# Kernel tuning notes

Measured on AMD Instinct MI355X. Metric: run time of the kernel, lower is better.

## Reference

```python
import jax, jax.numpy as jnp
import numpy as np

EPS = 1e-5

def _rms(t, w):
    # RMSNorm over last dim with learned scale w (broadcastable)
    return t * jax.lax.rsqrt(jnp.mean(t * t, axis=-1, keepdims=True) + EPS) * w

def setup_inputs() -> dict:
    key = jax.random.key(0)
    ks = jax.random.split(key, 8)
    B, S, D, H, HD, M = 2, 2048, 1024, 16, 64, 2
    E = H * HD
    sc = 0.02
    x = jax.random.normal(ks[0], (B, S, D), jnp.float32)
    attn_mask = jnp.zeros((S, S), jnp.float32)  # additive mask
    mod_ids = jax.random.randint(ks[1], (B, S), 0, M)
    Wq = jax.random.normal(ks[2], (M, D, E), jnp.float32) * sc
    Wk = jax.random.normal(ks[3], (M, D, E), jnp.float32) * sc
    Wv = jax.random.normal(ks[4], (M, D, E), jnp.float32) * sc
    Wo = jax.random.normal(ks[5], (M, E, D), jnp.float32) * sc
    qn_w = jnp.ones((M, HD), jnp.float32)
    kn_w = jnp.ones((M, HD), jnp.float32)
    attn_norm_w = jnp.ones((M, D), jnp.float32)
    return {"x": x, "attn_mask": attn_mask, "mod_ids": mod_ids,
            "Wq": Wq, "Wk": Wk, "Wv": Wv, "Wo": Wo,
            "qn_w": qn_w, "kn_w": kn_w, "attn_norm_w": attn_norm_w}

def reference(x, attn_mask, mod_ids, Wq, Wk, Wv, Wo, qn_w, kn_w, attn_norm_w):
    B, S, D = x.shape
    M = Wq.shape[0]
    HD = qn_w.shape[-1]
    E = Wq.shape[-1]
    H = E // HD
    msk = jax.nn.one_hot(mod_ids, M, dtype=x.dtype)  # [B,S,M] one-hot routing

    # modality-expert QKV projections: [M,B,S,E]
    q_m = jnp.einsum('bsd,mde->mbse', x, Wq).reshape(M, B, S, H, HD)
    k_m = jnp.einsum('bsd,mde->mbse', x, Wk).reshape(M, B, S, H, HD)
    v_m = jnp.einsum('bsd,mde->mbse', x, Wv)
    # per-modality, per-head QK RMSNorm
    q_m = _rms(q_m, qn_w[:, None, None, None, :]).reshape(M, B, S, E)
    k_m = _rms(k_m, kn_w[:, None, None, None, :]).reshape(M, B, S, E)

    # merge modalities (scatter by routing mask)
    q = jnp.einsum('bsm,mbse->bse', msk, q_m).reshape(B, S, H, HD)
    k = jnp.einsum('bsm,mbse->bse', msk, k_m).reshape(B, S, H, HD)
    v = jnp.einsum('bsm,mbse->bse', msk, v_m).reshape(B, S, H, HD)

    # standard multi-head attention
    scores = jnp.einsum('bqhd,bkhd->bhqk', q, k) / jnp.sqrt(jnp.asarray(HD, x.dtype))
    scores = scores + attn_mask  # additive mask broadcast over [B,H]
    attn = jax.nn.softmax(scores, axis=-1)
    ctx = jnp.einsum('bhqk,bkhd->bqhd', attn, v).reshape(B, S, E)
    attn_weights = attn.mean(axis=1)  # [B,S,S], averaged over heads

    # modality-expert output projection + RMSNorm, scatter-merge back
    o_m = jnp.einsum('bse,med->mbsd', ctx, Wo)
    o_m = _rms(o_m, attn_norm_w[:, None, None, :])
    out = jnp.einsum('bsm,mbsd->bsd', msk, o_m)
    return out, attn_weights
```

## Files before the change

kernel.cpp:

```cpp
#include <hip/hip_runtime.h>
#include <cstdint>

#define Bc  2
#define Sc  2048
#define Dc  1024
#define Ec  1024
#define Hc  16
#define HDc 64
#define TTc (Bc*Sc)
#define TILE_R 128
#define NTILES 36
#define EPSc 1e-5f
#define LOG2E 1.44269504f
#define C2    (0.125f*LOG2E)

typedef unsigned short u16;
using bf8   = __attribute__((ext_vector_type(8))) short;
using f32x4 = __attribute__((ext_vector_type(4))) float;
#define MFMA(a,b,c) __builtin_amdgcn_mfma_f32_16x16x32_bf16(a,b,c,0,0,0)

static __device__ __forceinline__ u16 f2b(float f){
    return (u16)((__float_as_uint(f) + 0x8000u) >> 16);
}
static __device__ __forceinline__ float b2f(u16 s){
    return __uint_as_float(((unsigned)s) << 16);
}
static __device__ __forceinline__ float ex2(float x){
    return __builtin_amdgcn_exp2f(x);
}
static __device__ __forceinline__ unsigned cvtpk(float a, float b){
    unsigned r;
    asm("v_cvt_pk_bf16_f32 %0, %1, %2" : "=v"(r) : "v"(a), "v"(b));
    return r;
}
union bfpack { unsigned u[4]; bf8 v; };
static __device__ __forceinline__ u16* swz(u16* base, int row, int col8){
    return base + row*64 + ((col8 ^ (row & 7)) << 3);
}
static __device__ __forceinline__ const u16* swzc(const u16* base, int row, int col8){
    return base + row*64 + ((col8 ^ (row & 7)) << 3);
}
typedef const __attribute__((address_space(1))) void* gp1;
typedef __attribute__((address_space(3))) void* lp3;
static __device__ __forceinline__ void gl16(const void* g, void* l){
    __builtin_amdgcn_global_load_lds((gp1)g, (lp3)l, 16, 0, 0);
}

__global__ void k_perm(const int* __restrict__ mod, int* __restrict__ perm,
                       int* __restrict__ tmeta, u16* __restrict__ zbuf)
{
    __shared__ int cnt[4], segstart[4];
    int t = threadIdx.x;
    for (int i = t; i < 2048; i += 256) zbuf[i] = 0;
    if (t < 4) cnt[t] = 0;
    __syncthreads();
    for (int i = t; i < TTc; i += 256){
        int b = i >> 11; int m = mod[i];
        atomicAdd(&cnt[b*2+m], 1);
    }
    __syncthreads();
    if (t == 0){
        int off = 0;
        for (int i = 0; i < 4; i++){
            segstart[i] = off;
            int pad = ((cnt[i] + TILE_R - 1)/TILE_R)*TILE_R;
            for (int tt = off/TILE_R; tt < (off+pad)/TILE_R; tt++) tmeta[tt] = i;
            off += pad;
        }
        for (int tt = off/TILE_R; tt < NTILES; tt++) tmeta[tt] = -1;
    }
    __syncthreads();
    if (t < 4) cnt[t] = 0;
    for (int i = t; i < NTILES*TILE_R; i += 256) perm[i] = -1;
    __syncthreads();
    for (int i = t; i < TTc; i += 256){
        int b = i >> 11, s = i & 2047; int m = mod[i];
        int r = atomicAdd(&cnt[b*2+m], 1);
        perm[segstart[b*2+m] + r] = s;
    }
}

__global__ __launch_bounds__(256) void k_f2b(const float* __restrict__ src,
                                             u16* __restrict__ dst, int n)
{
    int i = (blockIdx.x*256 + threadIdx.x)*4;
    if (i >= n) return;
    float4 v = *(const float4*)&src[i];
    ushort4 o;
    o.x = f2b(v.x); o.y = f2b(v.y); o.z = f2b(v.z); o.w = f2b(v.w);
    *(ushort4*)&dst[i] = o;
}

__global__ __launch_bounds__(256) void k_f2bs(const float* __restrict__ src,
                                              u16* __restrict__ dst, int n, float sc)
{
    int i = (blockIdx.x*256 + threadIdx.x)*4;
    if (i >= n) return;
    float4 v = *(const float4*)&src[i];
    ushort4 o;
    o.x = f2b(v.x*sc); o.y = f2b(v.y*sc); o.z = f2b(v.z*sc); o.w = f2b(v.w*sc);
    *(ushort4*)&dst[i] = o;
}

__global__ __launch_bounds__(256) void k_tcvt(
    const float* __restrict__ s0, const float* __restrict__ s1,
    const float* __restrict__ s2, const float* __restrict__ s3,
    u16* __restrict__ d0, u16* __restrict__ d1,
    u16* __restrict__ d2, u16* __restrict__ d3)
{
    int wsel = blockIdx.z >> 1, m = blockIdx.z & 1;
    const float* src = (wsel==0?s0:wsel==1?s1:wsel==2?s2:s3) + (size_t)m*1048576;
    u16*       dst = (wsel==0?d0:wsel==1?d1:wsel==2?d2:d3) + (size_t)m*1048576;
    __shared__ float sh[32][33];
    int t = threadIdx.x;
    int i0 = blockIdx.x*32, j0 = blockIdx.y*32;
    {
        int i = t >> 3, j4 = (t & 7)*4;
        *(float4*)&sh[i][j4] = *(const float4*)&src[(size_t)(i0+i)*1024 + j0 + j4];
    }
    __syncthreads();
    {
        int j = t >> 3, i4 = (t & 7)*4;
        ushort4 o;
        o.x = f2b(sh[i4+0][j]); o.y = f2b(sh[i4+1][j]);
        o.z = f2b(sh[i4+2][j]); o.w = f2b(sh[i4+3][j]);
        *(ushort4*)&dst[(size_t)(j0+j)*1024 + i0 + i4] = o;
    }
}

__global__ __launch_bounds__(256) void k_qkv(
    const u16* __restrict__ xb, const u16* __restrict__ wqT,
    const u16* __restrict__ wkT, const u16* __restrict__ wvT,
    const int* __restrict__ perm, const int* __restrict__ tmeta,
    const float* __restrict__ qnw, const float* __restrict__ knw,
    const u16* __restrict__ zbuf,
    u16* __restrict__ qb, u16* __restrict__ kb, u16* __restrict__ vb)
{
    int meta = tmeta[blockIdx.y];
    if (meta < 0) return;
    int b = meta >> 1, m = meta & 1;
    const u16* W = (blockIdx.z==0 ? wqT : (blockIdx.z==1 ? wkT : wvT)) + (size_t)m*Ec*Dc;
    u16* outp    = (blockIdx.z==0 ? qb  : (blockIdx.z==1 ? kb  : vb));
    int c0 = blockIdx.x*128;
    int t = threadIdx.x, lane = t & 63, wv_ = t >> 6;
    int quad = lane >> 4, lc = lane & 15;

    __shared__ u16 at[128*64];
    __shared__ u16 bt[128*64];
    __shared__ int sperm[128];
    if (t < 128) sperm[t] = perm[blockIdx.y*128 + t];
    f32x4 acc[2][8];
    #pragma unroll
    for (int i=0;i<2;i++)
        #pragma unroll
        for (int j=0;j<8;j++) acc[i][j] = (f32x4){0.f,0.f,0.f,0.f};
    __syncthreads();

    int colsw = ((lane & 7) ^ (lane >> 3)) << 3;
    const u16* ab[4]; const u16* bb[4];
    #pragma unroll
    for (int i = 0; i < 4; i++){
        int row = wv_*32 + i*8 + (lane >> 3);
        int s_ = sperm[row];
        ab[i] = (s_ >= 0) ? (xb + ((size_t)(b*Sc + s_))*Dc + colsw) : zbuf;
        bb[i] = W + (size_t)(c0 + row)*Dc + colsw;
    }

    for (int d0 = 0; d0 < Dc; d0 += 64){
        #pragma unroll
        for (int i = 0; i < 4; i++){
            gl16(ab[i] + d0, &at[(wv_*4 + i)*512]);
            gl16(bb[i] + d0, &bt[(wv_*4 + i)*512]);
        }
        __syncthreads();
        #pragma unroll
        for (int ks = 0; ks < 2; ks++){
            bf8 a0 = *(const bf8*)swzc(at, wv_*32 + lc,      ks*4 + quad);
            bf8 a1 = *(const bf8*)swzc(at, wv_*32 + 16 + lc, ks*4 + quad);
            #pragma unroll
            for (int nb = 0; nb < 8; nb++){
                bf8 bb2 = *(const bf8*)swzc(bt, nb*16 + lc, ks*4 + quad);
                acc[0][nb] = MFMA(a0, bb2, acc[0][nb]);
                acc[1][nb] = MFMA(a1, bb2, acc[1][nb]);
            }
        }
        __syncthreads();
    }

    if (blockIdx.z < 2){
        const float* nw = (blockIdx.z==0 ? qnw : knw) + m*HDc;
        float cs = (blockIdx.z==0) ? C2 : 1.f;
        float w0 = nw[lc]*cs, w1 = nw[16+lc]*cs, w2 = nw[32+lc]*cs, w3 = nw[48+lc]*cs;
        #pragma unroll
        for (int mb = 0; mb < 2; mb++){
            #pragma unroll
            for (int r = 0; r < 4; r++){
                #pragma unroll
                for (int g = 0; g < 2; g++){
                    float ss = 0.f;
                    #pragma unroll
                    for (int j = 0; j < 4; j++){
                        float v2 = acc[mb][g*4+j][r];
                        ss += v2*v2;
                    }
                    ss += __shfl_xor(ss, 1, 64);
                    ss += __shfl_xor(ss, 2, 64);
                    ss += __shfl_xor(ss, 4, 64);
                    ss += __shfl_xor(ss, 8, 64);
                    float rs = rsqrtf(ss*(1.f/64.f) + EPSc);
                    acc[mb][g*4+0][r] *= rs*w0;
                    acc[mb][g*4+1][r] *= rs*w1;
                    acc[mb][g*4+2][r] *= rs*w2;
                    acc[mb][g*4+3][r] *= rs*w3;
                }
            }
        }
    }

    int h0 = c0 >> 6;
    #pragma unroll
    for (int mb = 0; mb < 2; mb++){
        #pragma unroll
        for (int r = 0; r < 4; r++){
            int row = wv_*32 + mb*16 + quad*4 + r;
            int s_ = sperm[row];
            if (s_ < 0) continue;
            #pragma unroll
            for (int nb = 0; nb < 8; nb++){
                int col = nb*16 + lc;
                int h = h0 + (col >> 6), hd = col & 63;
                outp[(((size_t)(b*Hc + h))*Sc + s_)*HDc + hd] = f2b(acc[mb][nb][r]);
            }
        }
    }
}

__global__ __launch_bounds__(256) void k_vt(const u16* __restrict__ vb,
                                            u16* __restrict__ vtb)
{
    __shared__ u16 sh[64][72];
    int t = threadIdx.x;
    int s0 = blockIdx.x*64, bh = blockIdx.y;
    {
        int rr = t >> 2, cc = (t & 3)*16;
        const u16* src = vb + ((size_t)bh*Sc + s0 + rr)*HDc + cc;
        *(uint4*)&sh[rr][cc]   = *(const uint4*)(src);
        *(uint4*)&sh[rr][cc+8] = *(const uint4*)(src+8);
    }
    __syncthreads();
    {
        int hd = t >> 2, sc = (t & 3)*16;
        u16 tmp[16];
        #pragma unroll
        for (int j = 0; j < 16; j++) tmp[j] = sh[sc+j][hd];
        u16* dst = vtb + ((size_t)bh*HDc + hd)*Sc + s0 + sc;
        *(uint4*)(dst)   = *(const uint4*)&tmp[0];
        *(uint4*)(dst+8) = *(const uint4*)&tmp[8];
    }
}

__global__ __launch_bounds__(256) void k_flash(
    const u16* __restrict__ qb, const u16* __restrict__ kb,
    const u16* __restrict__ vtb, const u16* __restrict__ maskb,
    float* __restrict__ pm, float* __restrict__ pl,
    u16* __restrict__ c0, u16* __restrict__ c1)
{
    int qs0 = blockIdx.x*64, h = blockIdx.y;
    int b = blockIdx.z >> 1, half = blockIdx.z & 1;
    u16* ctxh = half ? c1 : c0;
    int t = threadIdx.x, lane = t & 63, wv_ = t >> 6;
    int quad = lane >> 4, lc = lane & 15;
    __shared__ u16 kt[64*64];
    __shared__ u16 vt[64*64];
    const u16* qp  = qb  + ((size_t)(b*Hc+h))*Sc*HDc;
    const u16* kp  = kb  + ((size_t)(b*Hc+h))*Sc*HDc;
    const u16* vtp = vtb + ((size_t)(b*Hc+h))*HDc*Sc;
    const u16* mq  = maskb + (size_t)(qs0 + wv_*16 + lc)*Sc;
    bf8 aq[2];
    #pragma unroll
    for (int ks = 0; ks < 2; ks++)
        aq[ks] = *(const bf8*)(qp + (size_t)(qs0 + wv_*16 + lc)*HDc + ks*32 + quad*8);
    float rm = -1.0e30f, rl = 0.f;
    f32x4 oacc[4];
    #pragma unroll
    for (int j=0;j<4;j++) oacc[j] = (f32x4){0.f,0.f,0.f,0.f};

    int rr = t >> 2, c8 = (t & 3)*2;
    int pr = (rr & 0x23) | ((rr & 0x04) << 2) | ((rr & 0x18) >> 1);
    int kc0 = half*1024;
    for (int kc = kc0; kc < kc0 + 1024; kc += 64){
        ushort4 mv[2][2];
        #pragma unroll
        for (int a1 = 0; a1 < 2; a1++)
            #pragma unroll
            for (int b1 = 0; b1 < 2; b1++)
                mv[a1][b1] = *(const ushort4*)(mq + kc + a1*32 + quad*8 + b1*4);
        __syncthreads();
        {
            const u16* s1 = kp + (size_t)(kc+rr)*HDc + c8*8;
            *(uint4*)swz(kt, pr, c8)   = *(const uint4*)(s1);
            *(uint4*)swz(kt, pr, c8+1) = *(const uint4*)(s1+8);
            const u16* s2 = vtp + (size_t)rr*Sc + kc + c8*8;
            *(uint4*)swz(vt, rr, c8)   = *(const uint4*)(s2);
            *(uint4*)swz(vt, rr, c8+1) = *(const uint4*)(s2+8);
        }
        __syncthreads();
        f32x4 acc[4];
        #pragma unroll
        for (int j=0;j<4;j++) acc[j] = (f32x4){0.f,0.f,0.f,0.f};
        #pragma unroll
        for (int ks = 0; ks < 2; ks++){
            #pragma unroll
            for (int nb = 0; nb < 4; nb++){
                bf8 ak = *(const bf8*)swzc(kt, nb*16 + lc, ks*4 + quad);
                acc[nb] = MFMA(ak, aq[ks], acc[nb]);
            }
        }
        float svv[4][4];
        float mxl = -3.0e38f;
        #pragma unroll
        for (int a1 = 0; a1 < 2; a1++){
            #pragma unroll
            for (int b1 = 0; b1 < 2; b1++){
                int nb = 2*a1 + b1;
                #pragma unroll
                for (int r = 0; r < 4; r++){
                    u16 mraw = (r==0?mv[a1][b1].x:r==1?mv[a1][b1].y:
                                r==2?mv[a1][b1].z:mv[a1][b1].w);
                    float s2v = acc[nb][r] + b2f(mraw);
                    svv[nb][r] = s2v;
                    mxl = fmaxf(mxl, s2v);
                }
            }
        }
        if (__any(mxl > rm + 8.f)){
            float mx = fmaxf(mxl, __shfl_xor(mxl, 16, 64));
            mx = fmaxf(mx, __shfl_xor(mx, 32, 64));
            float nm = fmaxf(rm, mx);
            float fac = ex2(rm - nm);
            rm = nm;
            rl *= fac;
            float f0 = __shfl(fac, quad*4+0, 64);
            float f1 = __shfl(fac, quad*4+1, 64);
            float f2 = __shfl(fac, quad*4+2, 64);
            float f3 = __shfl(fac, quad*4+3, 64);
            #pragma unroll
            for (int nb = 0; nb < 4; nb++){
                oacc[nb][0] *= f0; oacc[nb][1] *= f1;
                oacc[nb][2] *= f2; oacc[nb][3] *= f3;
            }
        }
        #pragma unroll
        for (int a1 = 0; a1 < 2; a1++){
            bfpack pk;
            {
                float p0 = ex2(svv[2*a1][0] - rm);
                float p1 = ex2(svv[2*a1][1] - rm);
                float p2 = ex2(svv[2*a1][2] - rm);
                float p3 = ex2(svv[2*a1][3] - rm);
                rl += (p0 + p1) + (p2 + p3);
                pk.u[0] = cvtpk(p0, p1); pk.u[1] = cvtpk(p2, p3);
            }
            {
                float p0 = ex2(svv[2*a1+1][0] - rm);
                float p1 = ex2(svv[2*a1+1][1] - rm);
                float p2 = ex2(svv[2*a1+1][2] - rm);
                float p3 = ex2(svv[2*a1+1][3] - rm);
                rl += (p0 + p1) + (p2 + p3);
                pk.u[2] = cvtpk(p0, p1); pk.u[3] = cvtpk(p2, p3);
            }
            bf8 ap = pk.v;
            #pragma unroll
            for (int nb2 = 0; nb2 < 4; nb2++){
                bf8 bv = *(const bf8*)swzc(vt, nb2*16 + lc, a1*4 + quad);
                oacc[nb2] = MFMA(ap, bv, oacc[nb2]);
            }
        }
    }
    rl += __shfl_xor(rl, 16, 64);
    rl += __shfl_xor(rl, 32, 64);
    if (quad == 0){
        size_t srow = ((size_t)(b*Hc+h))*Sc + qs0 + wv_*16 + lc;
        pm[(size_t)half*65536 + srow] = rm;
        pl[(size_t)half*65536 + srow] = rl;
    }
    float i0 = 1.f/__shfl(rl, quad*4+0, 64);
    float i1 = 1.f/__shfl(rl, quad*4+1, 64);
    float i2 = 1.f/__shfl(rl, quad*4+2, 64);
    float i3 = 1.f/__shfl(rl, quad*4+3, 64);
    #pragma unroll
    for (int r = 0; r < 4; r++){
        float ir = (r==0?i0:r==1?i1:r==2?i2:i3);
        int tok = qs0 + wv_*16 + quad*4 + r;
        #pragma unroll
        for (int nb = 0; nb < 4; nb++){
            int hd = nb*16 + lc;
            ctxh[((size_t)(b*Sc + tok))*Ec + h*HDc + hd] = f2b(oacc[nb][r]*ir);
        }
    }
}

__global__ __launch_bounds__(256) void k_merge(
    const float* __restrict__ pm, const float* __restrict__ pl,
    float* __restrict__ lstc, float* __restrict__ w0, float* __restrict__ w1)
{
    int r = blockIdx.x*256 + threadIdx.x;
    float m0 = pm[r],        m1 = pm[65536 + r];
    float l0 = pl[r],        l1 = pl[65536 + r];
    float M  = fmaxf(m0, m1);
    float e0 = ex2(m0 - M)*l0;
    float e1 = ex2(m1 - M)*l1;
    float L  = e0 + e1;
    float iL = 1.f/L;
    lstc[r] = M + log2f(L);
    w0[r] = e0*iL;
    w1[r] = e1*iL;
}

__global__ __launch_bounds__(256) void k_addc(u16* __restrict__ c0,
                                              const u16* __restrict__ c1,
                                              const float* __restrict__ w0,
                                              const float* __restrict__ w1)
{
    int i = (blockIdx.x*256 + threadIdx.x)*8;
    int hh = (i >> 6) & 15, s = (i >> 10) & 2047, bb = i >> 21;
    int wi = ((bb*Hc + hh) << 11) + s;
    float wa = w0[wi], wb = w1[wi];
    ushort4 a0 = *(ushort4*)&c0[i],   a1 = *(ushort4*)&c0[i+4];
    ushort4 b0 = *(const ushort4*)&c1[i], b1 = *(const ushort4*)&c1[i+4];
    ushort4 o0, o1;
    o0.x = f2b(b2f(a0.x)*wa + b2f(b0.x)*wb); o0.y = f2b(b2f(a0.y)*wa + b2f(b0.y)*wb);
    o0.z = f2b(b2f(a0.z)*wa + b2f(b0.z)*wb); o0.w = f2b(b2f(a0.w)*wa + b2f(b0.w)*wb);
    o1.x = f2b(b2f(a1.x)*wa + b2f(b1.x)*wb); o1.y = f2b(b2f(a1.y)*wa + b2f(b1.y)*wb);
    o1.z = f2b(b2f(a1.z)*wa + b2f(b1.z)*wb); o1.w = f2b(b2f(a1.w)*wa + b2f(b1.w)*wb);
    *(ushort4*)&c0[i]   = o0;
    *(ushort4*)&c0[i+4] = o1;
}

__global__ __launch_bounds__(256) void k_attnw(
    const u16* __restrict__ qb, const u16* __restrict__ kb,
    const u16* __restrict__ maskb, const float* __restrict__ lstc,
    float* __restrict__ awout)
{
    int qs0 = blockIdx.x*64, ks0 = blockIdx.y*64, b = blockIdx.z;
    int t = threadIdx.x, lane = t & 63, wv_ = t >> 6;
    int quad = lane >> 4, lc = lane & 15;
    __shared__ u16 kt[64*64];
    __shared__ float scc[64];
    f32x4 T[4];
    #pragma unroll
    for (int j=0;j<4;j++) T[j] = (f32x4){0.f,0.f,0.f,0.f};

    for (int h = 0; h < Hc; h++){
        __syncthreads();
        const u16* qp = qb + ((size_t)(b*Hc+h))*Sc*HDc;
        const u16* kp = kb + ((size_t)(b*Hc+h))*Sc*HDc;
        bf8 aq[2];
        #pragma unroll
        for (int ks = 0; ks < 2; ks++)
            aq[ks] = *(const bf8*)(qp + (size_t)(qs0 + wv_*16 + lc)*HDc + ks*32 + quad*8);
        {
            int rr = t >> 2, c8 = (t & 3)*2;
            const u16* s2 = kp + (size_t)(ks0+rr)*HDc + c8*8;
            *(uint4*)swz(kt, rr, c8)   = *(const uint4*)(s2);
            *(uint4*)swz(kt, rr, c8+1) = *(const uint4*)(s2+8);
        }
        if (t < 64)
            scc[t] = lstc[((size_t)(b*Hc+h))*Sc + qs0 + t];
        __syncthreads();
        f32x4 acc[4];
        #pragma unroll
        for (int j=0;j<4;j++) acc[j] = (f32x4){0.f,0.f,0.f,0.f};
        #pragma unroll
        for (int ks = 0; ks < 2; ks++){
            #pragma unroll
            for (int nb = 0; nb < 4; nb++){
                bf8 bb = *(const bf8*)swzc(kt, nb*16 + lc, ks*4 + quad);
                acc[nb] = MFMA(aq[ks], bb, acc[nb]);
            }
        }
        #pragma unroll
        for (int r = 0; r < 4; r++){
            int row = wv_*16 + quad*4 + r;
            float cv = scc[row];
            #pragma unroll
            for (int nb = 0; nb < 4; nb++)
                T[nb][r] += ex2(acc[nb][r] - cv);
        }
    }
    #pragma unroll
    for (int r = 0; r < 4; r++){
        int gq = qs0 + wv_*16 + quad*4 + r;
        #pragma unroll
        for (int nb = 0; nb < 4; nb++){
            int gk = ks0 + nb*16 + lc;
            float mk = b2f(maskb[(size_t)gq*Sc + gk]);
            awout[(size_t)b*Sc*Sc + (size_t)gq*Sc + gk]
                = T[nb][r]*ex2(mk)*(1.f/16.f);
        }
    }
}

__global__ __launch_bounds__(256) void k_oproj(
    const u16* __restrict__ ctxb, const u16* __restrict__ woT,
    const int* __restrict__ perm, const int* __restrict__ tmeta,
    const u16* __restrict__ zbuf, float* __restrict__ opre)
{
    int meta = tmeta[blockIdx.y];
    if (meta < 0) return;
    int b = meta >> 1, m = meta & 1;
    const u16* W = woT + (size_t)m*Ec*Dc;
    int c0 = blockIdx.x*128;
    int t = threadIdx.x, lane = t & 63, wv_ = t >> 6;
    int quad = lane >> 4, lc = lane & 15;
    __shared__ u16 at[128*64];
    __shared__ u16 bt[128*64];
    __shared__ int sperm[128];
    if (t < 128) sperm[t] = perm[blockIdx.y*128 + t];
    f32x4 acc[2][8];
    #pragma unroll
    for (int i=0;i<2;i++)
        #pragma unroll
        for (int j=0;j<8;j++) acc[i][j] = (f32x4){0.f,0.f,0.f,0.f};
    __syncthreads();

    int colsw = ((lane & 7) ^ (lane >> 3)) << 3;
    const u16* ab[4]; const u16* bb[4];
    #pragma unroll
    for (int i = 0; i < 4; i++){
        int row = wv_*32 + i*8 + (lane >> 3);
        int s_ = sperm[row];
        ab[i] = (s_ >= 0) ? (ctxb + ((size_t)(b*Sc + s_))*Ec + colsw) : zbuf;
        bb[i] = W + (size_t)(c0 + row)*Ec + colsw;
    }

    for (int d0 = 0; d0 < Ec; d0 += 64){
        #pragma unroll
        for (int i = 0; i < 4; i++){
            gl16(ab[i] + d0, &at[(wv_*4 + i)*512]);
            gl16(bb[i] + d0, &bt[(wv_*4 + i)*512]);
        }
        __syncthreads();
        #pragma unroll
        for (int ks = 0; ks < 2; ks++){
            bf8 a0 = *(const bf8*)swzc(at, wv_*32 + lc,      ks*4 + quad);
            bf8 a1 = *(const bf8*)swzc(at, wv_*32 + 16 + lc, ks*4 + quad);
            #pragma unroll
            for (int nb = 0; nb < 8; nb++){
                bf8 bb2 = *(const bf8*)swzc(bt, nb*16 + lc, ks*4 + quad);
                acc[0][nb] = MFMA(a0, bb2, acc[0][nb]);
                acc[1][nb] = MFMA(a1, bb2, acc[1][nb]);
            }
        }
        __syncthreads();
    }
    #pragma unroll
    for (int mb = 0; mb < 2; mb++){
        #pragma unroll
        for (int r = 0; r < 4; r++){
            int row = wv_*32 + mb*16 + quad*4 + r;
            int s_ = sperm[row];
            if (s_ < 0) continue;
            #pragma unroll
            for (int nb = 0; nb < 8; nb++){
                int col = c0 + nb*16 + lc;
                opre[((size_t)(b*Sc + s_))*Dc + col] = acc[mb][nb][r];
            }
        }
    }
}

__global__ __launch_bounds__(256) void k_onorm(
    const float* __restrict__ opre, const float* __restrict__ anw,
    const int* __restrict__ mod, float* __restrict__ out)
{
    int row = blockIdx.x;
    int m = mod[row];
    int t = threadIdx.x;
    float val[4];
    float ss = 0.f;
    #pragma unroll
    for (int j=0;j<4;j++){
        val[j] = opre[(size_t)row*Dc + t + 256*j];
        ss += val[j]*val[j];
    }
    #pragma unroll
    for (int o=32;o>0;o>>=1) ss += __shfl_xor(ss, o, 64);
    __shared__ float red[4];
    int wid = t>>6, lane = t&63;
    if (lane==0) red[wid]=ss;
    __syncthreads();
    float tot = red[0]+red[1]+red[2]+red[3];
    float rms = rsqrtf(tot*(1.f/1024.f) + EPSc);
    #pragma unroll
    for (int j=0;j<4;j++)
        out[(size_t)row*Dc + t + 256*j] = val[j]*rms*anw[m*Dc + t + 256*j];
}

extern "C" void kernel_launch(void* const* d_in, const int* in_sizes, int n_in,
                              void* d_out, int out_size, void* d_ws, size_t ws_size,
                              hipStream_t stream)
{
    const float* x    = (const float*)d_in[0];
    const float* mask = (const float*)d_in[1];
    const int*   mod  = (const int*)  d_in[2];
    const float* Wq   = (const float*)d_in[3];
    const float* Wk   = (const float*)d_in[4];
    const float* Wv   = (const float*)d_in[5];
    const float* Wo   = (const float*)d_in[6];
    const float* qnw  = (const float*)d_in[7];
    const float* knw  = (const float*)d_in[8];
    const float* anw  = (const float*)d_in[9];

    float* out   = (float*)d_out;
    float* awout = out + (size_t)Bc*Sc*Dc;

    float* ws = (float*)d_ws;
    u16* qb    = (u16*)(ws + 0);
    u16* kb    = (u16*)(ws + 2097152);
    u16* vb    = (u16*)(ws + 4194304);
    u16* xb    = (u16*)(ws + 6291456);
    u16* ctx0  = xb;
    u16* ctx1  = vb;
    u16* vtb   = (u16*)(ws + 8388608);
    u16* wqT   = (u16*)(ws + 10485760);
    u16* wkT   = (u16*)(ws + 11534336);
    u16* wvT   = (u16*)(ws + 12582912);
    u16* woT   = (u16*)(ws + 13631488);
    float* lstc= ws + 14680064;
    float* pm  = ws + 14811136;
    float* pl  = pm + 131072;
    float* w0  = ws + 15073280;
    float* w1  = w0 + 65536;
    u16* maskb = (u16*)(ws + 15335424);
    int* perm  = (int*)(ws + 17432576);
    int* tmeta = perm + NTILES*TILE_R;
    u16* zbuf  = (u16*)(tmeta + NTILES + 28);
    float* opre = ws;

    k_perm  <<<dim3(1),            256, 0, stream>>>(mod, perm, tmeta, zbuf);
    k_f2b   <<<dim3(4096),         256, 0, stream>>>(x, xb, Bc*Sc*Dc);
    k_f2bs  <<<dim3(4096),         256, 0, stream>>>(mask, maskb, Sc*Sc, LOG2E);
    k_tcvt  <<<dim3(32,32,8),      256, 0, stream>>>(Wq, Wk, Wv, Wo, wqT, wkT, wvT, woT);
    k_qkv   <<<dim3(8,NTILES,3),   256, 0, stream>>>(xb, wqT, wkT, wvT, perm, tmeta,
                                                     qnw, knw, zbuf, qb, kb, vb);
    k_vt    <<<dim3(32,32),        256, 0, stream>>>(vb, vtb);
    k_flash <<<dim3(32,16,4),      256, 0, stream>>>(qb, kb, vtb, maskb, pm, pl, ctx0, ctx1);
    k_merge <<<dim3(256),          256, 0, stream>>>(pm, pl, lstc, w0, w1);
    k_attnw <<<dim3(32,32,2),      256, 0, stream>>>(qb, kb, maskb, lstc, awout);
    k_addc  <<<dim3(2048),         256, 0, stream>>>(ctx0, ctx1, w0, w1);
    k_oproj <<<dim3(8,NTILES),     256, 0, stream>>>(ctx0, woT, perm, tmeta, zbuf, opre);
    k_onorm <<<dim3(4096),         256, 0, stream>>>(opre, anw, mod, out);
}
```

Before: 347.0 us.

## Use direct global-to-LDS loads in flash and attnw, MFMA row sums, fuse prep kernels

The K and V tile staging in the flash kernel and the K staging in the attention-weights kernel now use global_load_lds with the swizzle folded into the source addresses, replacing register-staged copies. The softmax row sum is computed by an MFMA against a vector of ones instead of scalar adds and cross-lane shuffles. The row-max reduction uses a max3 tree, and the two fp32-to-bf16 conversion kernels are merged into one launch. Together these aim to cut VGPR traffic, VALU work and launch overhead, but they change several parts at once. Summing the bf16-rounded probabilities also slightly changes the normaliser's numerics.

```diff
diff --git a/kernel.cpp b/kernel.cpp
--- a/kernel.cpp
+++ b/kernel.cpp
@@ -34,6 +34,9 @@
     return r;
 }
 union bfpack { unsigned u[4]; bf8 v; };
+static __device__ __forceinline__ float max3f(float a, float b, float c){
+    return fmaxf(fmaxf(a, b), c);
+}
 static __device__ __forceinline__ u16* swz(u16* base, int row, int col8){
     return base + row*64 + ((col8 ^ (row & 7)) << 3);
 }
@@ -44,6 +47,9 @@
 typedef __attribute__((address_space(3))) void* lp3;
 static __device__ __forceinline__ void gl16(const void* g, void* l){
     __builtin_amdgcn_global_load_lds((gp1)g, (lp3)l, 16, 0, 0);
+}
+static __device__ __forceinline__ int pinv(int lr){
+    return (lr & 0x23) | ((lr & 0x10) >> 2) | ((lr & 0x0C) << 1);
 }
 
 __global__ void k_perm(const int* __restrict__ mod, int* __restrict__ perm,
@@ -80,26 +86,25 @@
     }
 }
 
-__global__ __launch_bounds__(256) void k_f2b(const float* __restrict__ src,
-                                             u16* __restrict__ dst, int n)
-{
-    int i = (blockIdx.x*256 + threadIdx.x)*4;
-    if (i >= n) return;
-    float4 v = *(const float4*)&src[i];
-    ushort4 o;
-    o.x = f2b(v.x); o.y = f2b(v.y); o.z = f2b(v.z); o.w = f2b(v.w);
-    *(ushort4*)&dst[i] = o;
-}
-
-__global__ __launch_bounds__(256) void k_f2bs(const float* __restrict__ src,
-                                              u16* __restrict__ dst, int n, float sc)
-{
-    int i = (blockIdx.x*256 + threadIdx.x)*4;
-    if (i >= n) return;
-    float4 v = *(const float4*)&src[i];
-    ushort4 o;
-    o.x = f2b(v.x*sc); o.y = f2b(v.y*sc); o.z = f2b(v.z*sc); o.w = f2b(v.w*sc);
-    *(ushort4*)&dst[i] = o;
+__global__ __launch_bounds__(256) void k_prep(
+    const float* __restrict__ x, const float* __restrict__ mask,
+    u16* __restrict__ xb, u16* __restrict__ maskb)
+{
+    int bid = blockIdx.x;
+    if (bid < 4096){
+        int i = (bid*256 + threadIdx.x)*4;
+        float4 v = *(const float4*)&x[i];
+        ushort4 o;
+        o.x = f2b(v.x); o.y = f2b(v.y); o.z = f2b(v.z); o.w = f2b(v.w);
+        *(ushort4*)&xb[i] = o;
+    } else {
+        int i = ((bid-4096)*256 + threadIdx.x)*4;
+        float4 v = *(const float4*)&mask[i];
+        ushort4 o;
+        o.x = f2b(v.x*LOG2E); o.y = f2b(v.y*LOG2E);
+        o.z = f2b(v.z*LOG2E); o.w = f2b(v.w*LOG2E);
+        *(ushort4*)&maskb[i] = o;
+    }
 }
 
 __global__ __launch_bounds__(256) void k_tcvt(
@@ -280,13 +285,26 @@
     #pragma unroll
     for (int ks = 0; ks < 2; ks++)
         aq[ks] = *(const bf8*)(qp + (size_t)(qs0 + wv_*16 + lc)*HDc + ks*32 + quad*8);
-    float rm = -1.0e30f, rl = 0.f;
+    bfpack onep; onep.u[0] = onep.u[1] = onep.u[2] = onep.u[3] = 0x3F803F80u;
+    bf8 ones = onep.v;
+    float rm = -1.0e30f;
+    f32x4 racc = (f32x4){0.f,0.f,0.f,0.f};
     f32x4 oacc[4];
     #pragma unroll
     for (int j=0;j<4;j++) oacc[j] = (f32x4){0.f,0.f,0.f,0.f};
 
-    int rr = t >> 2, c8 = (t & 3)*2;
-    int pr = (rr & 0x23) | ((rr & 0x04) << 2) | ((rr & 0x18) >> 1);
+    int lsub = lane >> 3;
+    int colsw = ((lane & 7) ^ lsub) << 3;
+    int lrA = wv_*16 + lsub, lrB = wv_*16 + 8 + lsub;
+    const u16* kg0 = kp + (size_t)pinv(lrA)*HDc + colsw;
+    const u16* kg1 = kp + (size_t)pinv(lrB)*HDc + colsw;
+    const u16* vg0 = vtp + (size_t)lrA*Sc + colsw;
+    const u16* vg1 = vtp + (size_t)lrB*Sc + colsw;
+    u16* kd0 = &kt[(wv_*16 + 0)*64];
+    u16* kd1 = &kt[(wv_*16 + 8)*64];
+    u16* vd0 = &vt[(wv_*16 + 0)*64];
+    u16* vd1 = &vt[(wv_*16 + 8)*64];
+
     int kc0 = half*1024;
     for (int kc = kc0; kc < kc0 + 1024; kc += 64){
         ushort4 mv[2][2];
@@ -296,14 +314,10 @@
             for (int b1 = 0; b1 < 2; b1++)
                 mv[a1][b1] = *(const ushort4*)(mq + kc + a1*32 + quad*8 + b1*4);
         __syncthreads();
-        {
-            const u16* s1 = kp + (size_t)(kc+rr)*HDc + c8*8;
-            *(uint4*)swz(kt, pr, c8)   = *(const uint4*)(s1);
-            *(uint4*)swz(kt, pr, c8+1) = *(const uint4*)(s1+8);
-            const u16* s2 = vtp + (size_t)rr*Sc + kc + c8*8;
-            *(uint4*)swz(vt, rr, c8)   = *(const uint4*)(s2);
-            *(uint4*)swz(vt, rr, c8+1) = *(const uint4*)(s2+8);
-        }
+        gl16(kg0 + (size_t)kc*HDc, kd0);
+        gl16(kg1 + (size_t)kc*HDc, kd1);
+        gl16(vg0 + kc, vd0);
+        gl16(vg1 + kc, vd1);
         __syncthreads();
         f32x4 acc[4];
         #pragma unroll
@@ -317,7 +331,6 @@
             }
         }
         float svv[4][4];
-        float mxl = -3.0e38f;
         #pragma unroll
         for (int a1 = 0; a1 < 2; a1++){
             #pragma unroll
@@ -327,23 +340,27 @@
                 for (int r = 0; r < 4; r++){
                     u16 mraw = (r==0?mv[a1][b1].x:r==1?mv[a1][b1].y:
                                 r==2?mv[a1][b1].z:mv[a1][b1].w);
-                    float s2v = acc[nb][r] + b2f(mraw);
-                    svv[nb][r] = s2v;
-                    mxl = fmaxf(mxl, s2v);
+                    svv[nb][r] = acc[nb][r] + b2f(mraw);
                 }
             }
         }
+        float m0_ = max3f(svv[0][0], svv[0][1], svv[0][2]);
+        float m1_ = max3f(svv[0][3], svv[1][0], svv[1][1]);
+        float m2_ = max3f(svv[1][2], svv[1][3], svv[2][0]);
+        float m3_ = max3f(svv[2][1], svv[2][2], svv[2][3]);
+        float m4_ = max3f(svv[3][0], svv[3][1], svv[3][2]);
+        float mxl = fmaxf(max3f(m0_, m1_, m2_), max3f(m3_, m4_, svv[3][3]));
         if (__any(mxl > rm + 8.f)){
             float mx = fmaxf(mxl, __shfl_xor(mxl, 16, 64));
             mx = fmaxf(mx, __shfl_xor(mx, 32, 64));
             float nm = fmaxf(rm, mx);
             float fac = ex2(rm - nm);
             rm = nm;
-            rl *= fac;
             float f0 = __shfl(fac, quad*4+0, 64);
             float f1 = __shfl(fac, quad*4+1, 64);
             float f2 = __shfl(fac, quad*4+2, 64);
             float f3 = __shfl(fac, quad*4+3, 64);
+            racc[0] *= f0; racc[1] *= f1; racc[2] *= f2; racc[3] *= f3;
             #pragma unroll
             for (int nb = 0; nb < 4; nb++){
                 oacc[nb][0] *= f0; oacc[nb][1] *= f1;
@@ -353,23 +370,12 @@
         #pragma unroll
         for (int a1 = 0; a1 < 2; a1++){
             bfpack pk;
-            {
-                float p0 = ex2(svv[2*a1][0] - rm);
-                float p1 = ex2(svv[2*a1][1] - rm);
-                float p2 = ex2(svv[2*a1][2] - rm);
-                float p3 = ex2(svv[2*a1][3] - rm);
-                rl += (p0 + p1) + (p2 + p3);
-                pk.u[0] = cvtpk(p0, p1); pk.u[1] = cvtpk(p2, p3);
-            }
-            {
-                float p0 = ex2(svv[2*a1+1][0] - rm);
-                float p1 = ex2(svv[2*a1+1][1] - rm);
-                float p2 = ex2(svv[2*a1+1][2] - rm);
-                float p3 = ex2(svv[2*a1+1][3] - rm);
-                rl += (p0 + p1) + (p2 + p3);
-                pk.u[2] = cvtpk(p0, p1); pk.u[3] = cvtpk(p2, p3);
-            }
+            pk.u[0] = cvtpk(ex2(svv[2*a1][0] - rm),   ex2(svv[2*a1][1] - rm));
+            pk.u[1] = cvtpk(ex2(svv[2*a1][2] - rm),   ex2(svv[2*a1][3] - rm));
+            pk.u[2] = cvtpk(ex2(svv[2*a1+1][0] - rm), ex2(svv[2*a1+1][1] - rm));
+            pk.u[3] = cvtpk(ex2(svv[2*a1+1][2] - rm), ex2(svv[2*a1+1][3] - rm));
             bf8 ap = pk.v;
+            racc = MFMA(ap, ones, racc);
             #pragma unroll
             for (int nb2 = 0; nb2 < 4; nb2++){
                 bf8 bv = *(const bf8*)swzc(vt, nb2*16 + lc, a1*4 + quad);
@@ -377,20 +383,15 @@
             }
         }
     }
-    rl += __shfl_xor(rl, 16, 64);
-    rl += __shfl_xor(rl, 32, 64);
-    if (quad == 0){
-        size_t srow = ((size_t)(b*Hc+h))*Sc + qs0 + wv_*16 + lc;
-        pm[(size_t)half*65536 + srow] = rm;
-        pl[(size_t)half*65536 + srow] = rl;
-    }
-    float i0 = 1.f/__shfl(rl, quad*4+0, 64);
-    float i1 = 1.f/__shfl(rl, quad*4+1, 64);
-    float i2 = 1.f/__shfl(rl, quad*4+2, 64);
-    float i3 = 1.f/__shfl(rl, quad*4+3, 64);
+    size_t sbase = (size_t)half*65536 + ((size_t)(b*Hc+h))*Sc + qs0 + wv_*16;
+    if (quad == 0) pm[sbase + lc] = rm;
+    if (lc == 0){
+        #pragma unroll
+        for (int r = 0; r < 4; r++) pl[sbase + quad*4 + r] = racc[r];
+    }
     #pragma unroll
     for (int r = 0; r < 4; r++){
-        float ir = (r==0?i0:r==1?i1:r==2?i2:i3);
+        float ir = 1.f/racc[r];
         int tok = qs0 + wv_*16 + quad*4 + r;
         #pragma unroll
         for (int nb = 0; nb < 4; nb++){
@@ -451,6 +452,12 @@
     #pragma unroll
     for (int j=0;j<4;j++) T[j] = (f32x4){0.f,0.f,0.f,0.f};
 
+    int lsub = lane >> 3;
+    int colsw = ((lane & 7) ^ lsub) << 3;
+    int lrA = wv_*16 + lsub, lrB = wv_*16 + 8 + lsub;
+    u16* kd0 = &kt[(wv_*16 + 0)*64];
+    u16* kd1 = &kt[(wv_*16 + 8)*64];
+
     for (int h = 0; h < Hc; h++){
         __syncthreads();
         const u16* qp = qb + ((size_t)(b*Hc+h))*Sc*HDc;
@@ -459,12 +466,8 @@
         #pragma unroll
         for (int ks = 0; ks < 2; ks++)
             aq[ks] = *(const bf8*)(qp + (size_t)(qs0 + wv_*16 + lc)*HDc + ks*32 + quad*8);
-        {
-            int rr = t >> 2, c8 = (t & 3)*2;
-            const u16* s2 = kp + (size_t)(ks0+rr)*HDc + c8*8;
-            *(uint4*)swz(kt, rr, c8)   = *(const uint4*)(s2);
-            *(uint4*)swz(kt, rr, c8+1) = *(const uint4*)(s2+8);
-        }
+        gl16(kp + (size_t)(ks0 + lrA)*HDc + colsw, kd0);
+        gl16(kp + (size_t)(ks0 + lrB)*HDc + colsw, kd1);
         if (t < 64)
             scc[t] = lstc[((size_t)(b*Hc+h))*Sc + qs0 + t];
         __syncthreads();
@@ -639,8 +642,7 @@
     float* opre = ws;
 
     k_perm  <<<dim3(1),            256, 0, stream>>>(mod, perm, tmeta, zbuf);
-    k_f2b   <<<dim3(4096),         256, 0, stream>>>(x, xb, Bc*Sc*Dc);
-    k_f2bs  <<<dim3(4096),         256, 0, stream>>>(mask, maskb, Sc*Sc, LOG2E);
+    k_prep  <<<dim3(8192),         256, 0, stream>>>(x, mask, xb, maskb);
     k_tcvt  <<<dim3(32,32,8),      256, 0, stream>>>(Wq, Wk, Wv, Wo, wqT, wkT, wvT, woT);
     k_qkv   <<<dim3(8,NTILES,3),   256, 0, stream>>>(xb, wqT, wkT, wvT, perm, tmeta,
                                                      qnw, knw, zbuf, qb, kb, vb);
```

After: 349.5 us. Within noise of the previous version (+0.7%).
